# Optimization experiments

Measured on AMD Instinct MI355X. Metric: run time of the kernel, lower is better.

## Reference

```python
import jax, jax.numpy as jnp
import numpy as np

N_HEADS = 16
N_CHANNELS = 1024
DIM_HEAD = N_CHANNELS // N_HEADS


def setup_inputs() -> dict:
    key = jax.random.key(0)
    k1, k2, k3, k4 = jax.random.split(key, 4)
    B, S, D = 4, 2048, N_CHANNELS
    x = jax.random.normal(k1, (B, S, D), dtype=jnp.float32)
    # in_proj: Linear(D, 3D, bias=False); torch weight shape [3D, D], y = x @ W.T
    w_in = jax.random.normal(k2, (3 * D, D), dtype=jnp.float32) * (1.0 / np.sqrt(D))
    # out_proj: Linear(D, D) with bias
    w_out = jax.random.normal(k3, (D, D), dtype=jnp.float32) * (1.0 / np.sqrt(D))
    b_out = jax.random.normal(k4, (D,), dtype=jnp.float32) * 0.01
    return {"x": x, "w_in": w_in, "w_out": w_out, "b_out": b_out}


def reference(x, w_in, w_out, b_out):
    B, S, D = x.shape
    H, Dh = N_HEADS, DIM_HEAD
    qkv = jnp.einsum('bsd,ed->bse', x, w_in)  # [B,S,3D]
    q, k, v = jnp.split(qkv, 3, axis=-1)
    # [B,S,D] -> [B,H,S,Dh]
    def to_heads(t):
        return t.reshape(B, S, H, Dh).transpose(0, 2, 1, 3)
    q, k, v = to_heads(q), to_heads(k), to_heads(v)
    scale = 1.0 / np.sqrt(Dh)
    scores = jnp.einsum('bhqd,bhkd->bhqk', q, k) * scale  # [B,H,S,S]
    attn = jax.nn.softmax(scores, axis=-1)
    out = jnp.einsum('bhqk,bhkd->bhqd', attn, v)  # [B,H,S,Dh]
    out = out.transpose(0, 2, 1, 3).reshape(B, S, D)
    return jnp.einsum('bsd,ed->bse', out, w_out) + b_out
```

## Files before the change

### kernel.cpp

```cpp
#include <hip/hip_runtime.h>

typedef __bf16 bf16;
typedef __bf16 bf16x2 __attribute__((ext_vector_type(2)));
typedef __bf16 bf16x4 __attribute__((ext_vector_type(4)));
typedef __bf16 bf16x8 __attribute__((ext_vector_type(8)));
typedef float f32x4 __attribute__((ext_vector_type(4)));

typedef __attribute__((address_space(1))) const unsigned int gq_t;
typedef __attribute__((address_space(3))) unsigned int lq_t;

__global__ __launch_bounds__(256) void cvt_bf16(const float* __restrict__ in,
                                                bf16* __restrict__ out,
                                                int n8) {
  int i = blockIdx.x * 256 + threadIdx.x;
  if (i >= n8) return;
  f32x4 a = ((const f32x4*)in)[2 * i];
  f32x4 b = ((const f32x4*)in)[2 * i + 1];
  bf16x8 o;
#pragma unroll
  for (int j = 0; j < 4; ++j) {
    o[j] = (bf16)a[j];
    o[4 + j] = (bf16)b[j];
  }
  ((bf16x8*)out)[i] = o;
}

template <typename TC, bool ADD_BIAS>
__global__ __launch_bounds__(256) void gemm_glds(const bf16* __restrict__ A,
                                                 const bf16* __restrict__ B,
                                                 const float* __restrict__ bias,
                                                 TC* __restrict__ C,
                                                 int M, int N, int K, int lda) {
  __shared__ __align__(16) bf16 As[128 * 64];
  __shared__ __align__(16) bf16 Bs[128 * 64];
  const int tid = threadIdx.x;
  const int lane = tid & 63;
  const int wid = tid >> 6;
  const int wr = wid >> 1, wc = wid & 1;
  const int m0 = blockIdx.y * 128;
  const int n0 = blockIdx.x * 128;
  const int l16 = lane & 15;
  const int lhi = lane >> 4;
  const int lr = lane >> 3;
  const int lc = (lane & 7) * 8;

  f32x4 acc[4][4] = {};

  for (int k0 = 0; k0 < K; k0 += 64) {
    __syncthreads();
#pragma unroll
    for (int i = 0; i < 4; ++i) {
      const int chunk = wid * 4 + i;
      const int row = chunk * 8 + lr;
      const bf16* ga = A + (size_t)(m0 + row) * lda + k0 + lc;
      const bf16* gb = B + (size_t)(n0 + row) * K + k0 + lc;
      __builtin_amdgcn_global_load_lds((gq_t*)ga, (lq_t*)&As[chunk * 512], 16,
                                       0, 0);
      __builtin_amdgcn_global_load_lds((gq_t*)gb, (lq_t*)&Bs[chunk * 512], 16,
                                       0, 0);
    }
    __syncthreads();
#pragma unroll
    for (int ks = 0; ks < 2; ++ks) {
      bf16x8 af[4], bfr[4];
#pragma unroll
      for (int i = 0; i < 4; ++i) {
        af[i] = *(const bf16x8*)(&As[(wr * 64 + i * 16 + l16) * 64 + ks * 32 +
                                     lhi * 8]);
        bfr[i] = *(const bf16x8*)(&Bs[(wc * 64 + i * 16 + l16) * 64 + ks * 32 +
                                      lhi * 8]);
      }
#pragma unroll
      for (int i = 0; i < 4; ++i)
#pragma unroll
        for (int j = 0; j < 4; ++j)
          acc[i][j] = __builtin_amdgcn_mfma_f32_16x16x32_bf16(af[i], bfr[j],
                                                              acc[i][j], 0, 0, 0);
    }
  }

#pragma unroll
  for (int i = 0; i < 4; ++i) {
    int row_base = m0 + wr * 64 + i * 16 + lhi * 4;
#pragma unroll
    for (int j = 0; j < 4; ++j) {
      int col = n0 + wc * 64 + j * 16 + l16;
      float bv = ADD_BIAS ? bias[col] : 0.0f;
#pragma unroll
      for (int r = 0; r < 4; ++r) {
        float val = acc[i][j][r] + bv;
        if constexpr (__is_same(TC, float))
          C[(size_t)(row_base + r) * N + col] = val;
        else
          C[(size_t)(row_base + r) * N + col] = (bf16)val;
      }
    }
  }
}

template <typename TA, typename TC, bool ADD_BIAS>
__global__ __launch_bounds__(256) void gemm_bt(const TA* __restrict__ A,
                                               const float* __restrict__ B,
                                               const float* __restrict__ bias,
                                               TC* __restrict__ C,
                                               int M, int N, int K,
                                               int lda, int row0) {
  __shared__ __align__(16) bf16 As[128][72];
  __shared__ __align__(16) bf16 Bs[128][72];
  const int tid = threadIdx.x;
  const int lane = tid & 63;
  const int wid = tid >> 6;
  const int wr = wid >> 1, wc = wid & 1;
  const int m0 = blockIdx.y * 128;
  const int n0 = blockIdx.x * 128;
  const int l16 = lane & 15;
  const int lhi = lane >> 4;

  f32x4 acc[4][4] = {};

  for (int k0 = 0; k0 < K; k0 += 64) {
    __syncthreads();
#pragma unroll
    for (int p = 0; p < 8; ++p) {
      int v = tid + p * 256;
      int row = v >> 4;
      int kc = (v & 15) * 4;
      size_t ai = (size_t)(row0 + m0 + row) * lda + k0 + kc;
      size_t bi = (size_t)(n0 + row) * K + k0 + kc;
      bf16x4 ab, bb;
      if constexpr (__is_same(TA, float)) {
        f32x4 a4 = *(const f32x4*)((const float*)A + ai);
#pragma unroll
        for (int j = 0; j < 4; ++j) ab[j] = (bf16)a4[j];
      } else {
        ab = *(const bf16x4*)((const bf16*)A + ai);
      }
      f32x4 b4 = *(const f32x4*)(B + bi);
#pragma unroll
      for (int j = 0; j < 4; ++j) bb[j] = (bf16)b4[j];
      *(bf16x4*)(&As[row][kc]) = ab;
      *(bf16x4*)(&Bs[row][kc]) = bb;
    }
    __syncthreads();
#pragma unroll
    for (int ks = 0; ks < 2; ++ks) {
      bf16x8 af[4], bfr[4];
#pragma unroll
      for (int i = 0; i < 4; ++i) {
        af[i] = *(const bf16x8*)(&As[wr * 64 + i * 16 + l16][ks * 32 + lhi * 8]);
        bfr[i] = *(const bf16x8*)(&Bs[wc * 64 + i * 16 + l16][ks * 32 + lhi * 8]);
      }
#pragma unroll
      for (int i = 0; i < 4; ++i)
#pragma unroll
        for (int j = 0; j < 4; ++j)
          acc[i][j] = __builtin_amdgcn_mfma_f32_16x16x32_bf16(af[i], bfr[j],
                                                              acc[i][j], 0, 0, 0);
    }
  }

#pragma unroll
  for (int i = 0; i < 4; ++i) {
    int row_base = m0 + wr * 64 + i * 16 + lhi * 4;
#pragma unroll
    for (int j = 0; j < 4; ++j) {
      int col = n0 + wc * 64 + j * 16 + l16;
      float bv = ADD_BIAS ? bias[col] : 0.0f;
#pragma unroll
      for (int r = 0; r < 4; ++r) {
        float val = acc[i][j][r] + bv;
        if constexpr (__is_same(TC, float))
          C[(size_t)(row_base + r) * N + col] = val;
        else
          C[(size_t)(row_base + r) * N + col] = (bf16)val;
      }
    }
  }
}

__global__ __launch_bounds__(256) void attn_fwd(bf16* __restrict__ qkv) {
  constexpr int S = 2048, D3 = 3072;
  constexpr float SCL = 0.18033688011112042f;
  constexpr float THR = 11.5f;
  __shared__ __align__(16) bf16 Kt[2][64][72];
  __shared__ __align__(16) bf16 Vt[2][64][72];
  __shared__ __align__(16) bf16 Pq[4][16][72];

  const int tid = threadIdx.x;
  const int lane = tid & 63;
  const int wid = tid >> 6;
  const int l16 = lane & 15, lhi = lane >> 4;

  const int nwg = gridDim.x * gridDim.y;
  const int bid = blockIdx.y * gridDim.x + blockIdx.x;
  const int swz = (bid & 7) * (nwg >> 3) + (bid >> 3);
  const int bh = swz >> 4;
  const int b = bh >> 4, h = bh & 15;
  const int q0 = (swz & 15) * 128 + wid * 32;

  bf16* base = qkv + (size_t)b * S * D3;
  bf16* qbase = base + h * 64;
  const bf16* kbase = base + 1024 + h * 64;
  const bf16* vbase = base + 2048 + h * 64;

  bf16x8 qfA[2], qfB[2];
#pragma unroll
  for (int ks = 0; ks < 2; ++ks) {
    qfA[ks] = *(const bf16x8*)(qbase + (size_t)(q0 + l16) * D3 + ks * 32 + lhi * 8);
    qfB[ks] = *(const bf16x8*)(qbase + (size_t)(q0 + 16 + l16) * D3 + ks * 32 + lhi * 8);
  }

  float mA = -1e30f, mB = -1e30f;
  float lA = 0.0f, lB = 0.0f;
  f32x4 oA[4] = {}, oB[4] = {};

  const int kp = tid & 31, oc = tid >> 5;

  {
    bf16x8 k0 = *(const bf16x8*)(kbase + (size_t)(2 * kp) * D3 + oc * 8);
    bf16x8 k1 = *(const bf16x8*)(kbase + (size_t)(2 * kp + 1) * D3 + oc * 8);
    bf16x8 v0 = *(const bf16x8*)(vbase + (size_t)(2 * kp) * D3 + oc * 8);
    bf16x8 v1 = *(const bf16x8*)(vbase + (size_t)(2 * kp + 1) * D3 + oc * 8);
    *(bf16x8*)(&Kt[0][2 * kp][oc * 8]) = k0;
    *(bf16x8*)(&Kt[0][2 * kp + 1][oc * 8]) = k1;
#pragma unroll
    for (int j = 0; j < 8; ++j) {
      bf16x2 pr;
      pr[0] = v0[j];
      pr[1] = v1[j];
      *(bf16x2*)(&Vt[0][oc * 8 + j][2 * kp]) = pr;
    }
  }
  __syncthreads();

  for (int t = 0; t < S; t += 64) {
    const int cur = (t >> 6) & 1;
    const bool havenext = (t + 64 < S);

    bf16x8 kn0, kn1, vn0, vn1;
    if (havenext) {
      const bf16* kb = kbase + (size_t)(t + 64) * D3;
      const bf16* vb = vbase + (size_t)(t + 64) * D3;
      kn0 = *(const bf16x8*)(kb + (size_t)(2 * kp) * D3 + oc * 8);
      kn1 = *(const bf16x8*)(kb + (size_t)(2 * kp + 1) * D3 + oc * 8);
      vn0 = *(const bf16x8*)(vb + (size_t)(2 * kp) * D3 + oc * 8);
      vn1 = *(const bf16x8*)(vb + (size_t)(2 * kp + 1) * D3 + oc * 8);
    }

    f32x4 scA[4] = {}, scB[4] = {};
    __builtin_amdgcn_s_setprio(1);
#pragma unroll
    for (int ct = 0; ct < 4; ++ct) {
#pragma unroll
      for (int ks = 0; ks < 2; ++ks) {
        bf16x8 kf = *(const bf16x8*)(&Kt[cur][ct * 16 + l16][ks * 32 + lhi * 8]);
        scA[ct] = __builtin_amdgcn_mfma_f32_16x16x32_bf16(kf, qfA[ks], scA[ct], 0, 0, 0);
        scB[ct] = __builtin_amdgcn_mfma_f32_16x16x32_bf16(kf, qfB[ks], scB[ct], 0, 0, 0);
      }
    }
    __builtin_amdgcn_s_setprio(0);

    {
      float cm[4];
#pragma unroll
      for (int ct = 0; ct < 4; ++ct)
        cm[ct] = fmaxf(fmaxf(scA[ct][0], scA[ct][1]), fmaxf(scA[ct][2], scA[ct][3]));
      float mxs = fmaxf(fmaxf(cm[0], cm[1]), fmaxf(cm[2], cm[3])) * SCL;
      if (!__all(mxs - mA <= THR)) {
        float mw = mxs;
        mw = fmaxf(mw, __shfl_xor(mw, 16));
        mw = fmaxf(mw, __shfl_xor(mw, 32));
        float nm = fmaxf(mA, mw);
        float alpha = __builtin_amdgcn_exp2f(mA - nm);
        mA = nm;
        lA *= alpha;
#pragma unroll
        for (int dt = 0; dt < 4; ++dt)
#pragma unroll
          for (int r = 0; r < 4; ++r) oA[dt][r] *= alpha;
      }
      float rs4[4];
#pragma unroll
      for (int ct = 0; ct < 4; ++ct) {
#pragma unroll
        for (int r = 0; r < 4; ++r) {
          float p = __builtin_amdgcn_exp2f(__builtin_fmaf(scA[ct][r], SCL, -mA));
          scA[ct][r] = p;
        }
        rs4[ct] = (scA[ct][0] + scA[ct][1]) + (scA[ct][2] + scA[ct][3]);
      }
      lA += (rs4[0] + rs4[1]) + (rs4[2] + rs4[3]);
    }
#pragma unroll
    for (int ct = 0; ct < 4; ++ct) {
      bf16x4 pk;
#pragma unroll
      for (int r = 0; r < 4; ++r) pk[r] = (bf16)scA[ct][r];
      *(bf16x4*)(&Pq[wid][l16][ct * 16 + lhi * 4]) = pk;
    }
    bf16x8 pfA0 = *(const bf16x8*)(&Pq[wid][l16][lhi * 8]);
    bf16x8 pfA1 = *(const bf16x8*)(&Pq[wid][l16][32 + lhi * 8]);

    {
      float cm[4];
#pragma unroll
      for (int ct = 0; ct < 4; ++ct)
        cm[ct] = fmaxf(fmaxf(scB[ct][0], scB[ct][1]), fmaxf(scB[ct][2], scB[ct][3]));
      float mxs = fmaxf(fmaxf(cm[0], cm[1]), fmaxf(cm[2], cm[3])) * SCL;
      if (!__all(mxs - mB <= THR)) {
        float mw = mxs;
        mw = fmaxf(mw, __shfl_xor(mw, 16));
        mw = fmaxf(mw, __shfl_xor(mw, 32));
        float nm = fmaxf(mB, mw);
        float alpha = __builtin_amdgcn_exp2f(mB - nm);
        mB = nm;
        lB *= alpha;
#pragma unroll
        for (int dt = 0; dt < 4; ++dt)
#pragma unroll
          for (int r = 0; r < 4; ++r) oB[dt][r] *= alpha;
      }
      float rs4[4];
#pragma unroll
      for (int ct = 0; ct < 4; ++ct) {
#pragma unroll
        for (int r = 0; r < 4; ++r) {
          float p = __builtin_amdgcn_exp2f(__builtin_fmaf(scB[ct][r], SCL, -mB));
          scB[ct][r] = p;
        }
        rs4[ct] = (scB[ct][0] + scB[ct][1]) + (scB[ct][2] + scB[ct][3]);
      }
      lB += (rs4[0] + rs4[1]) + (rs4[2] + rs4[3]);
    }
#pragma unroll
    for (int ct = 0; ct < 4; ++ct) {
      bf16x4 pk;
#pragma unroll
      for (int r = 0; r < 4; ++r) pk[r] = (bf16)scB[ct][r];
      *(bf16x4*)(&Pq[wid][l16][ct * 16 + lhi * 4]) = pk;
    }
    bf16x8 pfB0 = *(const bf16x8*)(&Pq[wid][l16][lhi * 8]);
    bf16x8 pfB1 = *(const bf16x8*)(&Pq[wid][l16][32 + lhi * 8]);

    if (havenext) {
      *(bf16x8*)(&Kt[cur ^ 1][2 * kp][oc * 8]) = kn0;
      *(bf16x8*)(&Kt[cur ^ 1][2 * kp + 1][oc * 8]) = kn1;
#pragma unroll
      for (int j = 0; j < 8; ++j) {
        bf16x2 pr;
        pr[0] = vn0[j];
        pr[1] = vn1[j];
        *(bf16x2*)(&Vt[cur ^ 1][oc * 8 + j][2 * kp]) = pr;
      }
    }

    __builtin_amdgcn_s_setprio(1);
#pragma unroll
    for (int dt = 0; dt < 4; ++dt) {
      bf16x8 vf0 = *(const bf16x8*)(&Vt[cur][dt * 16 + l16][lhi * 8]);
      bf16x8 vf1 = *(const bf16x8*)(&Vt[cur][dt * 16 + l16][32 + lhi * 8]);
      oA[dt] = __builtin_amdgcn_mfma_f32_16x16x32_bf16(vf0, pfA0, oA[dt], 0, 0, 0);
      oA[dt] = __builtin_amdgcn_mfma_f32_16x16x32_bf16(vf1, pfA1, oA[dt], 0, 0, 0);
      oB[dt] = __builtin_amdgcn_mfma_f32_16x16x32_bf16(vf0, pfB0, oB[dt], 0, 0, 0);
      oB[dt] = __builtin_amdgcn_mfma_f32_16x16x32_bf16(vf1, pfB1, oB[dt], 0, 0, 0);
    }
    __builtin_amdgcn_s_setprio(0);

    __syncthreads();
  }

  {
    float l_i = lA;
    l_i += __shfl_xor(l_i, 16);
    l_i += __shfl_xor(l_i, 32);
    float rl = 1.0f / l_i;
#pragma unroll
    for (int dt = 0; dt < 4; ++dt) {
      bf16x4 ok;
#pragma unroll
      for (int r = 0; r < 4; ++r) ok[r] = (bf16)(oA[dt][r] * rl);
      *(bf16x4*)(&Pq[wid][l16][dt * 16 + lhi * 4]) = ok;
    }
    bf16x8 r0 = *(const bf16x8*)(&Pq[wid][l16][lhi * 16]);
    bf16x8 r1 = *(const bf16x8*)(&Pq[wid][l16][lhi * 16 + 8]);
    bf16* orow = qbase + (size_t)(q0 + l16) * D3 + lhi * 16;
    *(bf16x8*)(orow) = r0;
    *(bf16x8*)(orow + 8) = r1;
  }
  {
    float l_i = lB;
    l_i += __shfl_xor(l_i, 16);
    l_i += __shfl_xor(l_i, 32);
    float rl = 1.0f / l_i;
#pragma unroll
    for (int dt = 0; dt < 4; ++dt) {
      bf16x4 ok;
#pragma unroll
      for (int r = 0; r < 4; ++r) ok[r] = (bf16)(oB[dt][r] * rl);
      *(bf16x4*)(&Pq[wid][l16][dt * 16 + lhi * 4]) = ok;
    }
    bf16x8 r0 = *(const bf16x8*)(&Pq[wid][l16][lhi * 16]);
    bf16x8 r1 = *(const bf16x8*)(&Pq[wid][l16][lhi * 16 + 8]);
    bf16* orow = qbase + (size_t)(q0 + 16 + l16) * D3 + lhi * 16;
    *(bf16x8*)(orow) = r0;
    *(bf16x8*)(orow + 8) = r1;
  }
}

extern "C" void kernel_launch(void* const* d_in, const int* in_sizes, int n_in,
                              void* d_out, int out_size, void* d_ws,
                              size_t ws_size, hipStream_t stream) {
  constexpr int B = 4, S = 2048, D = 1024;

  const float* x = nullptr;
  const float* w_in = nullptr;
  const float* w_out = nullptr;
  const float* b_out = nullptr;
  for (int i = 0; i < n_in; ++i) {
    switch (in_sizes[i]) {
      case 8388608: x = (const float*)d_in[i]; break;
      case 3145728: w_in = (const float*)d_in[i]; break;
      case 1048576: w_out = (const float*)d_in[i]; break;
      case 1024: b_out = (const float*)d_in[i]; break;
    }
  }
  float* out = (float*)d_out;

  bf16* qkv = (bf16*)d_ws;
  const size_t need_full = (size_t)B * S * 3 * D * 2;
  const size_t need_cvt = need_full +
                          ((size_t)B * S * D +
                           (size_t)3 * D * D +
                           (size_t)D * D) * 2;

  if (ws_size >= need_cvt) {
    bf16* xb = qkv + (size_t)B * S * 3 * D;
    bf16* w_inb = xb + (size_t)B * S * D;
    bf16* w_outb = w_inb + (size_t)3 * D * D;
    const int nx8 = B * S * D / 8;
    const int nwi8 = 3 * D * D / 8;
    const int nwo8 = D * D / 8;
    cvt_bf16<<<dim3((nx8 + 255) / 256), 256, 0, stream>>>(x, xb, nx8);
    cvt_bf16<<<dim3((nwi8 + 255) / 256), 256, 0, stream>>>(w_in, w_inb, nwi8);
    cvt_bf16<<<dim3((nwo8 + 255) / 256), 256, 0, stream>>>(w_out, w_outb, nwo8);

    gemm_glds<bf16, false><<<dim3(3 * D / 128, B * S / 128), 256, 0, stream>>>(
        xb, w_inb, nullptr, qkv, B * S, 3 * D, D, D);
    attn_fwd<<<dim3(S / 128, B * 16), 256, 0, stream>>>(qkv);
    gemm_glds<float, true><<<dim3(D / 128, B * S / 128), 256, 0, stream>>>(
        qkv, w_outb, b_out, out, B * S, D, D, 3 * D);
  } else if (ws_size >= need_full) {
    gemm_bt<float, bf16, false><<<dim3(3 * D / 128, B * S / 128), 256, 0,
                                  stream>>>(x, w_in, nullptr, qkv, B * S,
                                            3 * D, D, D, 0);
    attn_fwd<<<dim3(S / 128, B * 16), 256, 0, stream>>>(qkv);
    gemm_bt<bf16, float, true><<<dim3(D / 128, B * S / 128), 256, 0, stream>>>(
        qkv, w_out, b_out, out, B * S, D, D, 3 * D, 0);
  } else {
    for (int b0 = 0; b0 < B; ++b0) {
      gemm_bt<float, bf16, false><<<dim3(3 * D / 128, S / 128), 256, 0,
                                    stream>>>(x, w_in, nullptr, qkv, S, 3 * D,
                                              D, D, b0 * S);
      attn_fwd<<<dim3(S / 128, 16), 256, 0, stream>>>(qkv);
      gemm_bt<bf16, float, true><<<dim3(D / 128, S / 128), 256, 0, stream>>>(
          qkv, w_out, b_out, out + (size_t)b0 * S * D, S, D, D, 3 * D, 0);
    }
  }
}
```

Baseline: 328.2 us.

## Double-buffer LDS tiles in GEMM to overlap global loads with MFMA

```diff
diff --git a/kernel.cpp b/kernel.cpp
--- a/kernel.cpp
+++ b/kernel.cpp
@@ -31,8 +31,8 @@
                                                  const float* __restrict__ bias,
                                                  TC* __restrict__ C,
                                                  int M, int N, int K, int lda) {
-  __shared__ __align__(16) bf16 As[128 * 64];
-  __shared__ __align__(16) bf16 Bs[128 * 64];
+  __shared__ __align__(16) bf16 As[2][128 * 64];
+  __shared__ __align__(16) bf16 Bs[2][128 * 64];
   const int tid = threadIdx.x;
   const int lane = tid & 63;
   const int wid = tid >> 6;
@@ -46,37 +46,57 @@
 
   f32x4 acc[4][4] = {};
 
+#pragma unroll
+  for (int i = 0; i < 4; ++i) {
+    const int chunk = wid * 4 + i;
+    const int row = chunk * 8 + lr;
+    const bf16* ga = A + (size_t)(m0 + row) * lda + lc;
+    const bf16* gb = B + (size_t)(n0 + row) * K + lc;
+    __builtin_amdgcn_global_load_lds((gq_t*)ga, (lq_t*)&As[0][chunk * 512], 16,
+                                     0, 0);
+    __builtin_amdgcn_global_load_lds((gq_t*)gb, (lq_t*)&Bs[0][chunk * 512], 16,
+                                     0, 0);
+  }
+  __syncthreads();
+
+  int cur = 0;
   for (int k0 = 0; k0 < K; k0 += 64) {
-    __syncthreads();
-#pragma unroll
-    for (int i = 0; i < 4; ++i) {
-      const int chunk = wid * 4 + i;
-      const int row = chunk * 8 + lr;
-      const bf16* ga = A + (size_t)(m0 + row) * lda + k0 + lc;
-      const bf16* gb = B + (size_t)(n0 + row) * K + k0 + lc;
-      __builtin_amdgcn_global_load_lds((gq_t*)ga, (lq_t*)&As[chunk * 512], 16,
-                                       0, 0);
-      __builtin_amdgcn_global_load_lds((gq_t*)gb, (lq_t*)&Bs[chunk * 512], 16,
-                                       0, 0);
-    }
-    __syncthreads();
+    if (k0 + 64 < K) {
+#pragma unroll
+      for (int i = 0; i < 4; ++i) {
+        const int chunk = wid * 4 + i;
+        const int row = chunk * 8 + lr;
+        const bf16* ga = A + (size_t)(m0 + row) * lda + k0 + 64 + lc;
+        const bf16* gb = B + (size_t)(n0 + row) * K + k0 + 64 + lc;
+        __builtin_amdgcn_global_load_lds((gq_t*)ga,
+                                         (lq_t*)&As[cur ^ 1][chunk * 512], 16,
+                                         0, 0);
+        __builtin_amdgcn_global_load_lds((gq_t*)gb,
+                                         (lq_t*)&Bs[cur ^ 1][chunk * 512], 16,
+                                         0, 0);
+      }
+    }
 #pragma unroll
     for (int ks = 0; ks < 2; ++ks) {
       bf16x8 af[4], bfr[4];
 #pragma unroll
       for (int i = 0; i < 4; ++i) {
-        af[i] = *(const bf16x8*)(&As[(wr * 64 + i * 16 + l16) * 64 + ks * 32 +
-                                     lhi * 8]);
-        bfr[i] = *(const bf16x8*)(&Bs[(wc * 64 + i * 16 + l16) * 64 + ks * 32 +
-                                      lhi * 8]);
-      }
+        af[i] = *(const bf16x8*)(&As[cur][(wr * 64 + i * 16 + l16) * 64 +
+                                          ks * 32 + lhi * 8]);
+        bfr[i] = *(const bf16x8*)(&Bs[cur][(wc * 64 + i * 16 + l16) * 64 +
+                                           ks * 32 + lhi * 8]);
+      }
+      __builtin_amdgcn_s_setprio(1);
 #pragma unroll
       for (int i = 0; i < 4; ++i)
 #pragma unroll
         for (int j = 0; j < 4; ++j)
           acc[i][j] = __builtin_amdgcn_mfma_f32_16x16x32_bf16(af[i], bfr[j],
                                                               acc[i][j], 0, 0, 0);
-    }
+      __builtin_amdgcn_s_setprio(0);
+    }
+    __syncthreads();
+    cur ^= 1;
   }
 
 #pragma unroll
```

Measured after the change: 315.6 us. 1.04x faster.

## Replace GEMM with 256x128 tile, 8-wave triple-buffered ping-pong pipeline

Applied to the files above, without the earlier changes.

```diff
diff --git a/kernel.cpp b/kernel.cpp
--- a/kernel.cpp
+++ b/kernel.cpp
@@ -26,65 +26,120 @@
 }
 
 template <typename TC, bool ADD_BIAS>
-__global__ __launch_bounds__(256) void gemm_glds(const bf16* __restrict__ A,
-                                                 const bf16* __restrict__ B,
-                                                 const float* __restrict__ bias,
-                                                 TC* __restrict__ C,
-                                                 int M, int N, int K, int lda) {
-  __shared__ __align__(16) bf16 As[128 * 64];
-  __shared__ __align__(16) bf16 Bs[128 * 64];
+__global__ __launch_bounds__(512) void gemm_8ph(const bf16* __restrict__ A,
+                                                const bf16* __restrict__ B,
+                                                const float* __restrict__ bias,
+                                                TC* __restrict__ C,
+                                                int M, int N, int K, int lda) {
+  __shared__ __align__(16) bf16 As[3][256 * 64];
+  __shared__ __align__(16) bf16 Bs[3][128 * 64];
   const int tid = threadIdx.x;
   const int lane = tid & 63;
   const int wid = tid >> 6;
-  const int wr = wid >> 1, wc = wid & 1;
-  const int m0 = blockIdx.y * 128;
+  const int wm = wid >> 2;
+  const int wn = wid & 3;
+  const int m0 = blockIdx.y * 256;
   const int n0 = blockIdx.x * 128;
   const int l16 = lane & 15;
   const int lhi = lane >> 4;
   const int lr = lane >> 3;
   const int lc = (lane & 7) * 8;
 
-  f32x4 acc[4][4] = {};
-
-  for (int k0 = 0; k0 < K; k0 += 64) {
-    __syncthreads();
-#pragma unroll
-    for (int i = 0; i < 4; ++i) {
-      const int chunk = wid * 4 + i;
-      const int row = chunk * 8 + lr;
-      const bf16* ga = A + (size_t)(m0 + row) * lda + k0 + lc;
-      const bf16* gb = B + (size_t)(n0 + row) * K + k0 + lc;
-      __builtin_amdgcn_global_load_lds((gq_t*)ga, (lq_t*)&As[chunk * 512], 16,
-                                       0, 0);
-      __builtin_amdgcn_global_load_lds((gq_t*)gb, (lq_t*)&Bs[chunk * 512], 16,
-                                       0, 0);
-    }
-    __syncthreads();
-#pragma unroll
-    for (int ks = 0; ks < 2; ++ks) {
-      bf16x8 af[4], bfr[4];
-#pragma unroll
-      for (int i = 0; i < 4; ++i) {
-        af[i] = *(const bf16x8*)(&As[(wr * 64 + i * 16 + l16) * 64 + ks * 32 +
-                                     lhi * 8]);
-        bfr[i] = *(const bf16x8*)(&Bs[(wc * 64 + i * 16 + l16) * 64 + ks * 32 +
-                                      lhi * 8]);
-      }
-#pragma unroll
-      for (int i = 0; i < 4; ++i)
-#pragma unroll
-        for (int j = 0; j < 4; ++j)
-          acc[i][j] = __builtin_amdgcn_mfma_f32_16x16x32_bf16(af[i], bfr[j],
-                                                              acc[i][j], 0, 0, 0);
-    }
-  }
-
-#pragma unroll
-  for (int i = 0; i < 4; ++i) {
-    int row_base = m0 + wr * 64 + i * 16 + lhi * 4;
-#pragma unroll
-    for (int j = 0; j < 4; ++j) {
-      int col = n0 + wc * 64 + j * 16 + l16;
+  const int nkt = K >> 6;
+
+  f32x4 acc[8][2] = {};
+
+  auto stageA = [&](int kt, int buf, int u) {
+    const int chunk = wid * 4 + u;
+    const int row = chunk * 8 + lr;
+    const bf16* g = A + (size_t)(m0 + row) * lda + kt * 64 + lc;
+    __builtin_amdgcn_global_load_lds((gq_t*)g, (lq_t*)&As[buf][chunk * 512],
+                                     16, 0, 0);
+  };
+  auto stageB = [&](int kt, int buf, int u) {
+    const int chunk = wid * 2 + u;
+    const int row = chunk * 8 + lr;
+    const bf16* g = B + (size_t)(n0 + row) * K + kt * 64 + lc;
+    __builtin_amdgcn_global_load_lds((gq_t*)g, (lq_t*)&Bs[buf][chunk * 512],
+                                     16, 0, 0);
+  };
+
+  stageA(0, 0, 0); stageA(0, 0, 1); stageA(0, 0, 2); stageA(0, 0, 3);
+  stageB(0, 0, 0); stageB(0, 0, 1);
+  stageA(1, 1, 0); stageA(1, 1, 1); stageA(1, 1, 2); stageA(1, 1, 3);
+  stageB(1, 1, 0); stageB(1, 1, 1);
+  asm volatile("s_waitcnt vmcnt(6)" ::: "memory");
+  __builtin_amdgcn_sched_barrier(0);
+  __builtin_amdgcn_s_barrier();
+
+  for (int g = 0; g < nkt; ++g) {
+    const int buf = g % 3;
+    const int nbuf = (g + 2) % 3;
+    const bool donext = (g + 2) < nkt;
+    const bf16* Asb = &As[buf][0];
+    const bf16* Bsb = &Bs[buf][0];
+
+#pragma unroll
+    for (int q = 0; q < 4; ++q) {
+      const int mh = q >> 1, nh = q & 1;
+      bf16x8 af[4][2], bfn[2];
+#pragma unroll
+      for (int mf = 0; mf < 4; ++mf) {
+        const int mrow = wm * 128 + (mh * 4 + mf) * 16 + l16;
+#pragma unroll
+        for (int ks = 0; ks < 2; ++ks)
+          af[mf][ks] = *(const bf16x8*)(Asb + mrow * 64 + ks * 32 + lhi * 8);
+      }
+      {
+        const int nrow = wn * 32 + nh * 16 + l16;
+#pragma unroll
+        for (int ks = 0; ks < 2; ++ks)
+          bfn[ks] = *(const bf16x8*)(Bsb + nrow * 64 + ks * 32 + lhi * 8);
+      }
+      if (donext) {
+        if (q == 0) {
+          stageA(g + 2, nbuf, 0);
+          stageA(g + 2, nbuf, 1);
+        } else if (q == 1) {
+          stageA(g + 2, nbuf, 2);
+          stageA(g + 2, nbuf, 3);
+        } else if (q == 2) {
+          stageB(g + 2, nbuf, 0);
+        } else {
+          stageB(g + 2, nbuf, 1);
+        }
+      }
+      __builtin_amdgcn_s_barrier();
+      asm volatile("s_waitcnt lgkmcnt(0)" ::: "memory");
+      __builtin_amdgcn_sched_barrier(0);
+      __builtin_amdgcn_s_setprio(1);
+#pragma unroll
+      for (int mf = 0; mf < 4; ++mf)
+#pragma unroll
+        for (int ks = 0; ks < 2; ++ks)
+          acc[mh * 4 + mf][nh] = __builtin_amdgcn_mfma_f32_16x16x32_bf16(
+              af[mf][ks], bfn[ks], acc[mh * 4 + mf][nh], 0, 0, 0);
+      __builtin_amdgcn_s_setprio(0);
+      __builtin_amdgcn_s_barrier();
+    }
+
+    if (g + 1 < nkt) {
+      if (donext) {
+        asm volatile("s_waitcnt vmcnt(6)" ::: "memory");
+      } else {
+        asm volatile("s_waitcnt vmcnt(0)" ::: "memory");
+      }
+      __builtin_amdgcn_sched_barrier(0);
+      __builtin_amdgcn_s_barrier();
+    }
+  }
+
+#pragma unroll
+  for (int i = 0; i < 8; ++i) {
+    int row_base = m0 + wm * 128 + i * 16 + lhi * 4;
+#pragma unroll
+    for (int j = 0; j < 2; ++j) {
+      int col = n0 + wn * 32 + j * 16 + l16;
       float bv = ADD_BIAS ? bias[col] : 0.0f;
 #pragma unroll
       for (int r = 0; r < 4; ++r) {
@@ -444,10 +499,10 @@
     cvt_bf16<<<dim3((nwi8 + 255) / 256), 256, 0, stream>>>(w_in, w_inb, nwi8);
     cvt_bf16<<<dim3((nwo8 + 255) / 256), 256, 0, stream>>>(w_out, w_outb, nwo8);
 
-    gemm_glds<bf16, false><<<dim3(3 * D / 128, B * S / 128), 256, 0, stream>>>(
+    gemm_8ph<bf16, false><<<dim3(3 * D / 128, B * S / 256), 512, 0, stream>>>(
         xb, w_inb, nullptr, qkv, B * S, 3 * D, D, D);
     attn_fwd<<<dim3(S / 128, B * 16), 256, 0, stream>>>(qkv);
-    gemm_glds<float, true><<<dim3(D / 128, B * S / 128), 256, 0, stream>>>(
+    gemm_8ph<float, true><<<dim3(D / 128, B * S / 256), 512, 0, stream>>>(
         qkv, w_outb, b_out, out, B * S, D, D, 3 * D);
   } else if (ws_size >= need_full) {
     gemm_bt<float, bf16, false><<<dim3(3 * D / 128, B * S / 128), 256, 0,
```

Result: slower. 413.7 us (+26.1%).
